# Performance work log

Measured on AMD Instinct MI355X. Metric: run time of the kernel, lower is better.

Reference implementation:

```python
import jax, jax.numpy as jnp
import numpy as np
import math

B, T, D, H = 2, 2048, 1024, 16
DH = D // H

def setup_inputs() -> dict:
    key = jax.random.key(0)
    ks = jax.random.split(key, 7)
    s = 0.02
    return {
        "q": jax.random.normal(ks[0], (B, T, D), jnp.float32),
        "k": jax.random.normal(ks[1], (B, T, D), jnp.float32),
        "v": jax.random.normal(ks[2], (B, T, D), jnp.float32),
        "wq": jax.random.normal(ks[3], (D, D), jnp.float32) * s,
        "wk": jax.random.normal(ks[4], (D, D), jnp.float32) * s,
        "wv": jax.random.normal(ks[5], (D, D), jnp.float32) * s,
        "wo": jax.random.normal(ks[6], (D, D), jnp.float32) * s,
    }

def reference(q, k, v, wq, wk, wv, wo):
    # nn.Linear(bias=False): y = x @ W.T
    qh = (q @ wq.T).reshape(B, T, H, DH).transpose(0, 2, 1, 3)  # [B,H,T,DH]
    kh = (k @ wk.T).reshape(B, T, H, DH).transpose(0, 2, 1, 3)
    vh = (v @ wv.T).reshape(B, T, H, DH).transpose(0, 2, 1, 3)
    scores = jnp.einsum('bhqd,bhkd->bhqk', qh, kh) / math.sqrt(DH)
    # causal mask: disallow j > i
    mask = jnp.triu(jnp.ones((T, T), dtype=bool), k=1)
    scores = jnp.where(mask[None, None], -jnp.inf, scores)
    attn = jax.nn.softmax(scores, axis=-1)  # dropout=0 (eval)
    out = jnp.einsum('bhqk,bhkd->bhqd', attn, vh)
    out = out.transpose(0, 2, 1, 3).reshape(B, T, D)
    return out @ wo.T
```

## Files before the change

kernel.cpp:

```cpp
#include <hip/hip_runtime.h>
#include <cstdint>
#include <cstddef>

#define B_  2
#define T_  2048
#define D_  1024
#define H_  16
#define DH_ 64
#define M_  (B_*T_)

typedef __bf16 bf16x8 __attribute__((ext_vector_type(8)));
typedef float  f32x4  __attribute__((ext_vector_type(4)));
typedef unsigned short us4 __attribute__((ext_vector_type(4)));
typedef unsigned short us8 __attribute__((ext_vector_type(8)));
typedef unsigned short ushort_t;

__device__ __forceinline__ unsigned short f32_to_bf16_rne(float f) {
    unsigned u = __builtin_bit_cast(unsigned, f);
    u += 0x7FFFu + ((u >> 16) & 1u);
    return (unsigned short)(u >> 16);
}

__device__ __forceinline__ void async16(const void* g, void* l) {
    __builtin_amdgcn_global_load_lds(
        (const __attribute__((address_space(1))) unsigned int*)(uintptr_t)g,
        (__attribute__((address_space(3))) unsigned int*)(uintptr_t)l, 16, 0, 0);
}

__global__ __launch_bounds__(256) void cvt_qkv(const float* __restrict__ a, const float* __restrict__ b,
                                               const float* __restrict__ c,
                                               ushort_t* __restrict__ oa, ushort_t* __restrict__ ob,
                                               ushort_t* __restrict__ oc) {
    const float* in = blockIdx.y == 0 ? a : blockIdx.y == 1 ? b : c;
    ushort_t* out   = blockIdx.y == 0 ? oa : blockIdx.y == 1 ? ob : oc;
    int i = (blockIdx.x * 256 + threadIdx.x) * 4;
    float4 f = *reinterpret_cast<const float4*>(in + i);
    us4 o;
    o[0] = f32_to_bf16_rne(f.x); o[1] = f32_to_bf16_rne(f.y);
    o[2] = f32_to_bf16_rne(f.z); o[3] = f32_to_bf16_rne(f.w);
    *reinterpret_cast<us4*>(out + i) = o;
}

__global__ __launch_bounds__(256) void cvt_w(const float* __restrict__ a, const float* __restrict__ b,
                                             const float* __restrict__ c, const float* __restrict__ d,
                                             ushort_t* __restrict__ oa, ushort_t* __restrict__ ob,
                                             ushort_t* __restrict__ oc, ushort_t* __restrict__ od) {
    const float* in = blockIdx.y == 0 ? a : blockIdx.y == 1 ? b : blockIdx.y == 2 ? c : d;
    ushort_t* out   = blockIdx.y == 0 ? oa : blockIdx.y == 1 ? ob : blockIdx.y == 2 ? oc : od;
    int i = (blockIdx.x * 256 + threadIdx.x) * 4;
    float4 f = *reinterpret_cast<const float4*>(in + i);
    us4 o;
    o[0] = f32_to_bf16_rne(f.x); o[1] = f32_to_bf16_rne(f.y);
    o[2] = f32_to_bf16_rne(f.z); o[3] = f32_to_bf16_rne(f.w);
    *reinterpret_cast<us4*>(out + i) = o;
}

__device__ __forceinline__ void gemm_mainloop(const ushort_t* __restrict__ A,
                                              const ushort_t* __restrict__ W,
                                              ushort_t* As, ushort_t* Bs,
                                              int m0, int n0, f32x4 acc[4][4]) {
    const int tid  = threadIdx.x;
    const int lc   = tid & 15;
    const int quad = (tid >> 4) & 3;
    const int wave = tid >> 6;
    const int wm = (wave >> 1) * 64, wn = (wave & 1) * 64;

    const f32x4 fzero = {0.f, 0.f, 0.f, 0.f};
#pragma unroll
    for (int mt = 0; mt < 4; ++mt)
#pragma unroll
        for (int nt = 0; nt < 4; ++nt) acc[mt][nt] = fzero;

    for (int kk = 0; kk < D_; kk += 32) {
        __syncthreads();
#pragma unroll
        for (int i = 0; i < 2; ++i) {
            const int j = i * 256 + tid;
            async16(A + (size_t)(m0 + (j >> 2)) * D_ + kk + (j & 3) * 8, As + j * 8);
            async16(W + (size_t)(n0 + (j >> 2)) * D_ + kk + (j & 3) * 8, Bs + j * 8);
        }
        __syncthreads();
        bf16x8 af[4], bw[4];
#pragma unroll
        for (int mt = 0; mt < 4; ++mt)
            af[mt] = *reinterpret_cast<const bf16x8*>(As + (wm + mt * 16 + lc) * 32 + quad * 8);
#pragma unroll
        for (int nt = 0; nt < 4; ++nt)
            bw[nt] = *reinterpret_cast<const bf16x8*>(Bs + (wn + nt * 16 + lc) * 32 + quad * 8);
#pragma unroll
        for (int mt = 0; mt < 4; ++mt)
#pragma unroll
            for (int nt = 0; nt < 4; ++nt)
                acc[mt][nt] = __builtin_amdgcn_mfma_f32_16x16x32_bf16(af[mt], bw[nt], acc[mt][nt], 0, 0, 0);
    }
}

__global__ __launch_bounds__(256, 2) void gemm_qkv(
    const ushort_t* __restrict__ qb, const ushort_t* __restrict__ kb, const ushort_t* __restrict__ vb,
    const ushort_t* __restrict__ wqb, const ushort_t* __restrict__ wkb, const ushort_t* __restrict__ wvb,
    ushort_t* __restrict__ qhb, ushort_t* __restrict__ khb, ushort_t* __restrict__ vtb) {
    __shared__ __align__(16) ushort_t As[128 * 32];
    __shared__ __align__(16) ushort_t Bs[128 * 32];
    __shared__ __align__(16) ushort_t Ts[4][64 * 16];

    const int z = blockIdx.z;
    const ushort_t* A = z == 0 ? qb : z == 1 ? kb : vb;
    const ushort_t* W = z == 0 ? wqb : z == 1 ? wkb : wvb;
    const int m0 = blockIdx.y * 128, n0 = blockIdx.x * 128;

    f32x4 acc[4][4];
    gemm_mainloop(A, W, As, Bs, m0, n0, acc);

    const int tid = threadIdx.x, lane = tid & 63, lc = tid & 15;
    const int quad = (tid >> 4) & 3, wave = tid >> 6;
    const int wm = (wave >> 1) * 64, wn = (wave & 1) * 64;

    if (z < 2) {
        ushort_t* outp = z == 0 ? qhb : khb;
#pragma unroll
        for (int mt = 0; mt < 4; ++mt)
#pragma unroll
            for (int nt = 0; nt < 4; ++nt)
#pragma unroll
                for (int r = 0; r < 4; ++r) {
                    const int m = m0 + wm + mt * 16 + quad * 4 + r;
                    const int n = n0 + wn + nt * 16 + lc;
                    const int bb = m >> 11, t = m & (T_ - 1);
                    const int hh = n >> 6,  d = n & 63;
                    outp[(((size_t)bb * H_ + hh) * T_ + t) * DH_ + d] = f32_to_bf16_rne(acc[mt][nt][r]);
                }
    } else {
        const int mG = m0 + wm;
        const int bb = mG >> 11, t0 = mG & (T_ - 1);
        const int nG = n0 + wn, hh = nG >> 6;
        ushort_t* base = vtb + ((size_t)bb * H_ + hh) * DH_ * T_;
#pragma unroll
        for (int mt = 0; mt < 4; ++mt) {
#pragma unroll
            for (int nt = 0; nt < 4; ++nt)
#pragma unroll
                for (int r = 0; r < 4; ++r)
                    Ts[wave][(nt * 16 + lc) * 16 + quad * 4 + r] = f32_to_bf16_rne(acc[mt][nt][r]);
#pragma unroll
            for (int it = 0; it < 2; ++it) {
                const int c = it * 64 + lane;
                const int nl = c >> 1, mh = c & 1;
                us8 vv = *reinterpret_cast<const us8*>(Ts[wave] + c * 8);
                *reinterpret_cast<us8*>(base + (size_t)nl * T_ + t0 + mt * 16 + mh * 8) = vv;
            }
        }
    }
}

__global__ __launch_bounds__(256, 2) void gemm_wo(const ushort_t* __restrict__ A,
                                                  const ushort_t* __restrict__ W,
                                                  float* __restrict__ out) {
    __shared__ __align__(16) ushort_t As[128 * 32];
    __shared__ __align__(16) ushort_t Bs[128 * 32];
    const int m0 = blockIdx.y * 128, n0 = blockIdx.x * 128;
    f32x4 acc[4][4];
    gemm_mainloop(A, W, As, Bs, m0, n0, acc);

    const int tid = threadIdx.x, lc = tid & 15;
    const int quad = (tid >> 4) & 3, wave = tid >> 6;
    const int wm = (wave >> 1) * 64, wn = (wave & 1) * 64;
#pragma unroll
    for (int mt = 0; mt < 4; ++mt)
#pragma unroll
        for (int nt = 0; nt < 4; ++nt)
#pragma unroll
            for (int r = 0; r < 4; ++r) {
                const int m = m0 + wm + mt * 16 + quad * 4 + r;
                const int n = n0 + wn + nt * 16 + lc;
                out[(size_t)m * D_ + n] = acc[mt][nt][r];
            }
}

__global__ __launch_bounds__(256, 2) void attn2(const ushort_t* __restrict__ Qh,
                                                const ushort_t* __restrict__ Kh,
                                                const ushort_t* __restrict__ Vt,
                                                ushort_t* __restrict__ Ao) {
    __shared__ __align__(16) ushort_t Ks[2][64 * 64];
    __shared__ __align__(16) ushort_t Vs[2][64 * 64];
    __shared__ __align__(16) ushort_t Ps[4][16 * 72];

    const int tid = threadIdx.x, lane = tid & 63, lc = tid & 15;
    const int quad = (tid >> 4) & 3, wave = tid >> 6;
    const int bh = blockIdx.y, bb = bh >> 4, hh = bh & 15;

    const ushort_t* Qp = Qh + (size_t)bh * T_ * DH_;
    const ushort_t* Kp = Kh + (size_t)bh * T_ * DH_;
    const ushort_t* Vp = Vt + (size_t)bh * DH_ * T_;
    const float SC2 = 0.18033688f;

    auto stage = [&](int buf, int kt) {
        const int k0s = kt * 64;
#pragma unroll
        for (int i = 0; i < 2; ++i) {
            const int j = i * 256 + tid;
            async16(Kp + (size_t)(k0s + (j >> 3)) * DH_ + (j & 7) * 8, Ks[buf] + j * 8);
            async16(Vp + (size_t)(j >> 3) * T_ + k0s + (j & 7) * 8,    Vs[buf] + j * 8);
        }
    };

    const f32x4 fzero = {0.f, 0.f, 0.f, 0.f};

    for (int pass = 0; pass < 2; ++pass) {
        const int qt = pass ? (31 - (int)blockIdx.x) : (int)blockIdx.x;
        const int q0 = qt * 64, nkt = qt + 1;
        const int mbase = q0 + wave * 16;

        const ushort_t* qrow = Qp + (size_t)(mbase + lc) * DH_ + quad * 8;
        bf16x8 aq0 = *reinterpret_cast<const bf16x8*>(qrow);
        bf16x8 aq1 = *reinterpret_cast<const bf16x8*>(qrow + 32);

        f32x4 o[4];
        float lsum[4];
#pragma unroll
        for (int ct = 0; ct < 4; ++ct) o[ct] = fzero;
#pragma unroll
        for (int r = 0; r < 4; ++r) lsum[r] = 0.f;

        __syncthreads();
        stage(0, 0);

        for (int kt = 0; kt < nkt; ++kt) {
            const int cur = kt & 1;
            __syncthreads();
            if (kt + 1 < nkt) stage(cur ^ 1, kt + 1);
            const int k0 = kt * 64;

            f32x4 s[4];
#pragma unroll
            for (int ct = 0; ct < 4; ++ct) {
                const ushort_t* kr = Ks[cur] + (ct * 16 + lc) * 64 + quad * 8;
                bf16x8 bk0 = *reinterpret_cast<const bf16x8*>(kr);
                bf16x8 bk1 = *reinterpret_cast<const bf16x8*>(kr + 32);
                s[ct] = __builtin_amdgcn_mfma_f32_16x16x32_bf16(aq0, bk0, fzero, 0, 0, 0);
                s[ct] = __builtin_amdgcn_mfma_f32_16x16x32_bf16(aq1, bk1, s[ct], 0, 0, 0);
            }

#pragma unroll
            for (int ct = 0; ct < 4; ++ct) {
                const int col = k0 + ct * 16 + lc;
#pragma unroll
                for (int r = 0; r < 4; ++r) {
                    const int row = mbase + quad * 4 + r;
                    const float e = (col <= row) ? __builtin_amdgcn_exp2f(s[ct][r] * SC2) : 0.f;
                    lsum[r] += e;
                    Ps[wave][(quad * 4 + r) * 72 + ct * 16 + lc] = f32_to_bf16_rne(e);
                }
            }
            bf16x8 ap0 = *reinterpret_cast<const bf16x8*>(Ps[wave] + lc * 72 + quad * 8);
            bf16x8 ap1 = *reinterpret_cast<const bf16x8*>(Ps[wave] + lc * 72 + 32 + quad * 8);

#pragma unroll
            for (int ct = 0; ct < 4; ++ct) {
                const ushort_t* vr = Vs[cur] + (ct * 16 + lc) * 64 + quad * 8;
                bf16x8 bv0 = *reinterpret_cast<const bf16x8*>(vr);
                bf16x8 bv1 = *reinterpret_cast<const bf16x8*>(vr + 32);
                o[ct] = __builtin_amdgcn_mfma_f32_16x16x32_bf16(ap0, bv0, o[ct], 0, 0, 0);
                o[ct] = __builtin_amdgcn_mfma_f32_16x16x32_bf16(ap1, bv1, o[ct], 0, 0, 0);
            }
        }

        float inv[4];
#pragma unroll
        for (int r = 0; r < 4; ++r) {
            float l = lsum[r];
#pragma unroll
            for (int d = 1; d < 16; d <<= 1) l += __shfl_xor(l, d);
            inv[r] = 1.0f / l;
        }
#pragma unroll
        for (int ct = 0; ct < 4; ++ct)
#pragma unroll
            for (int r = 0; r < 4; ++r) {
                const int rowq = mbase + quad * 4 + r;
                Ao[((size_t)bb * T_ + rowq) * D_ + hh * DH_ + ct * 16 + lc] =
                    f32_to_bf16_rne(o[ct][r] * inv[r]);
            }
    }
}

extern "C" void kernel_launch(void* const* d_in, const int* in_sizes, int n_in,
                              void* d_out, int out_size, void* d_ws, size_t ws_size,
                              hipStream_t stream) {
    const float* q  = (const float*)d_in[0];
    const float* k  = (const float*)d_in[1];
    const float* v  = (const float*)d_in[2];
    const float* wq = (const float*)d_in[3];
    const float* wk = (const float*)d_in[4];
    const float* wv = (const float*)d_in[5];
    const float* wo = (const float*)d_in[6];

    char* ws = (char*)d_ws;
    size_t off = 0;
    auto alloc = [&](size_t bytes) -> char* {
        char* p = ws + off;
        off += (bytes + 255) & ~(size_t)255;
        return p;
    };
    ushort_t* qb  = (ushort_t*)alloc((size_t)M_ * D_ * 2);
    ushort_t* kb  = (ushort_t*)alloc((size_t)M_ * D_ * 2);
    ushort_t* vb  = (ushort_t*)alloc((size_t)M_ * D_ * 2);
    ushort_t* wqb = (ushort_t*)alloc((size_t)D_ * D_ * 2);
    ushort_t* wkb = (ushort_t*)alloc((size_t)D_ * D_ * 2);
    ushort_t* wvb = (ushort_t*)alloc((size_t)D_ * D_ * 2);
    ushort_t* wob = (ushort_t*)alloc((size_t)D_ * D_ * 2);
    ushort_t* qhb = (ushort_t*)alloc((size_t)M_ * D_ * 2);
    ushort_t* khb = (ushort_t*)alloc((size_t)M_ * D_ * 2);
    ushort_t* vtb = (ushort_t*)alloc((size_t)M_ * D_ * 2);
    ushort_t* aob = (ushort_t*)alloc((size_t)M_ * D_ * 2);

    cvt_qkv<<<dim3(4096, 3), 256, 0, stream>>>(q, k, v, qb, kb, vb);
    cvt_w  <<<dim3(1024, 4), 256, 0, stream>>>(wq, wk, wv, wo, wqb, wkb, wvb, wob);

    gemm_qkv<<<dim3(8, 32, 3), 256, 0, stream>>>(qb, kb, vb, wqb, wkb, wvb, qhb, khb, vtb);

    attn2<<<dim3(16, 32), 256, 0, stream>>>(qhb, khb, vtb, aob);

    gemm_wo<<<dim3(8, 32), 256, 0, stream>>>(aob, wob, (float*)d_out);
}
```

Before: 223.6 us.

## Widen GEMM K-tile with XOR swizzle, split attention KV across wave groups

The two conversion kernels are merged into one launch, with an early exit for the smaller weight tensors. The GEMM main loop stages K=64 per iteration into XOR-swizzled LDS to cut barriers and bank conflicts, and the launch-bound occupancy hint is raised to 3. Attention now uses 512-thread blocks in which two groups of four waves each process alternate KV tiles from a paired double buffer. Their partial outputs and row sums are combined through shared memory at the end, and the P scratch is swizzled too. The cost is more LDS per block, an extra reduction step, and idle work for one group when the tile count is odd.

```diff
diff --git a/kernel.cpp b/kernel.cpp
--- a/kernel.cpp
+++ b/kernel.cpp
@@ -27,27 +27,21 @@
         (__attribute__((address_space(3))) unsigned int*)(uintptr_t)l, 16, 0, 0);
 }
 
-__global__ __launch_bounds__(256) void cvt_qkv(const float* __restrict__ a, const float* __restrict__ b,
-                                               const float* __restrict__ c,
-                                               ushort_t* __restrict__ oa, ushort_t* __restrict__ ob,
-                                               ushort_t* __restrict__ oc) {
-    const float* in = blockIdx.y == 0 ? a : blockIdx.y == 1 ? b : c;
-    ushort_t* out   = blockIdx.y == 0 ? oa : blockIdx.y == 1 ? ob : oc;
+__global__ __launch_bounds__(256) void cvt_all(
+    const float* __restrict__ i0, const float* __restrict__ i1, const float* __restrict__ i2,
+    const float* __restrict__ i3, const float* __restrict__ i4, const float* __restrict__ i5,
+    const float* __restrict__ i6,
+    ushort_t* __restrict__ o0, ushort_t* __restrict__ o1, ushort_t* __restrict__ o2,
+    ushort_t* __restrict__ o3, ushort_t* __restrict__ o4, ushort_t* __restrict__ o5,
+    ushort_t* __restrict__ o6) {
+    const int y = blockIdx.y;
+    const float* in = y == 0 ? i0 : y == 1 ? i1 : y == 2 ? i2 : y == 3 ? i3
+                    : y == 4 ? i4 : y == 5 ? i5 : i6;
+    ushort_t* out  = y == 0 ? o0 : y == 1 ? o1 : y == 2 ? o2 : y == 3 ? o3
+                    : y == 4 ? o4 : y == 5 ? o5 : o6;
+    const int n = (y < 3) ? (M_ * D_) : (D_ * D_);
     int i = (blockIdx.x * 256 + threadIdx.x) * 4;
-    float4 f = *reinterpret_cast<const float4*>(in + i);
-    us4 o;
-    o[0] = f32_to_bf16_rne(f.x); o[1] = f32_to_bf16_rne(f.y);
-    o[2] = f32_to_bf16_rne(f.z); o[3] = f32_to_bf16_rne(f.w);
-    *reinterpret_cast<us4*>(out + i) = o;
-}
-
-__global__ __launch_bounds__(256) void cvt_w(const float* __restrict__ a, const float* __restrict__ b,
-                                             const float* __restrict__ c, const float* __restrict__ d,
-                                             ushort_t* __restrict__ oa, ushort_t* __restrict__ ob,
-                                             ushort_t* __restrict__ oc, ushort_t* __restrict__ od) {
-    const float* in = blockIdx.y == 0 ? a : blockIdx.y == 1 ? b : blockIdx.y == 2 ? c : d;
-    ushort_t* out   = blockIdx.y == 0 ? oa : blockIdx.y == 1 ? ob : blockIdx.y == 2 ? oc : od;
-    int i = (blockIdx.x * 256 + threadIdx.x) * 4;
+    if (i >= n) return;
     float4 f = *reinterpret_cast<const float4*>(in + i);
     us4 o;
     o[0] = f32_to_bf16_rne(f.x); o[1] = f32_to_bf16_rne(f.y);
@@ -64,6 +58,7 @@
     const int quad = (tid >> 4) & 3;
     const int wave = tid >> 6;
     const int wm = (wave >> 1) * 64, wn = (wave & 1) * 64;
+    const int sw = lc & 7;
 
     const f32x4 fzero = {0.f, 0.f, 0.f, 0.f};
 #pragma unroll
@@ -71,36 +66,42 @@
 #pragma unroll
         for (int nt = 0; nt < 4; ++nt) acc[mt][nt] = fzero;
 
-    for (int kk = 0; kk < D_; kk += 32) {
-        __syncthreads();
-#pragma unroll
-        for (int i = 0; i < 2; ++i) {
+    for (int kk = 0; kk < D_; kk += 64) {
+        __syncthreads();
+#pragma unroll
+        for (int i = 0; i < 4; ++i) {
             const int j = i * 256 + tid;
-            async16(A + (size_t)(m0 + (j >> 2)) * D_ + kk + (j & 3) * 8, As + j * 8);
-            async16(W + (size_t)(n0 + (j >> 2)) * D_ + kk + (j & 3) * 8, Bs + j * 8);
-        }
-        __syncthreads();
-        bf16x8 af[4], bw[4];
-#pragma unroll
-        for (int mt = 0; mt < 4; ++mt)
-            af[mt] = *reinterpret_cast<const bf16x8*>(As + (wm + mt * 16 + lc) * 32 + quad * 8);
-#pragma unroll
-        for (int nt = 0; nt < 4; ++nt)
-            bw[nt] = *reinterpret_cast<const bf16x8*>(Bs + (wn + nt * 16 + lc) * 32 + quad * 8);
-#pragma unroll
-        for (int mt = 0; mt < 4; ++mt)
+            const int r = j >> 3, c = (j & 7) ^ (r & 7);
+            async16(A + (size_t)(m0 + r) * D_ + kk + c * 8, As + j * 8);
+            async16(W + (size_t)(n0 + r) * D_ + kk + c * 8, Bs + j * 8);
+        }
+        __syncthreads();
+#pragma unroll
+        for (int ks = 0; ks < 2; ++ks) {
+            bf16x8 af[4], bw[4];
+#pragma unroll
+            for (int mt = 0; mt < 4; ++mt)
+                af[mt] = *reinterpret_cast<const bf16x8*>(
+                    As + (wm + mt * 16 + lc) * 64 + (((ks * 4 + quad) ^ sw) * 8));
 #pragma unroll
             for (int nt = 0; nt < 4; ++nt)
-                acc[mt][nt] = __builtin_amdgcn_mfma_f32_16x16x32_bf16(af[mt], bw[nt], acc[mt][nt], 0, 0, 0);
+                bw[nt] = *reinterpret_cast<const bf16x8*>(
+                    Bs + (wn + nt * 16 + lc) * 64 + (((ks * 4 + quad) ^ sw) * 8));
+#pragma unroll
+            for (int mt = 0; mt < 4; ++mt)
+#pragma unroll
+                for (int nt = 0; nt < 4; ++nt)
+                    acc[mt][nt] = __builtin_amdgcn_mfma_f32_16x16x32_bf16(af[mt], bw[nt], acc[mt][nt], 0, 0, 0);
+        }
     }
 }
 
-__global__ __launch_bounds__(256, 2) void gemm_qkv(
+__global__ __launch_bounds__(256, 3) void gemm_qkv(
     const ushort_t* __restrict__ qb, const ushort_t* __restrict__ kb, const ushort_t* __restrict__ vb,
     const ushort_t* __restrict__ wqb, const ushort_t* __restrict__ wkb, const ushort_t* __restrict__ wvb,
     ushort_t* __restrict__ qhb, ushort_t* __restrict__ khb, ushort_t* __restrict__ vtb) {
-    __shared__ __align__(16) ushort_t As[128 * 32];
-    __shared__ __align__(16) ushort_t Bs[128 * 32];
+    __shared__ __align__(16) ushort_t As[128 * 64];
+    __shared__ __align__(16) ushort_t Bs[128 * 64];
     __shared__ __align__(16) ushort_t Ts[4][64 * 16];
 
     const int z = blockIdx.z;
@@ -152,11 +153,11 @@
     }
 }
 
-__global__ __launch_bounds__(256, 2) void gemm_wo(const ushort_t* __restrict__ A,
+__global__ __launch_bounds__(256, 3) void gemm_wo(const ushort_t* __restrict__ A,
                                                   const ushort_t* __restrict__ W,
                                                   float* __restrict__ out) {
-    __shared__ __align__(16) ushort_t As[128 * 32];
-    __shared__ __align__(16) ushort_t Bs[128 * 32];
+    __shared__ __align__(16) ushort_t As[128 * 64];
+    __shared__ __align__(16) ushort_t Bs[128 * 64];
     const int m0 = blockIdx.y * 128, n0 = blockIdx.x * 128;
     f32x4 acc[4][4];
     gemm_mainloop(A, W, As, Bs, m0, n0, acc);
@@ -176,39 +177,31 @@
             }
 }
 
-__global__ __launch_bounds__(256, 2) void attn2(const ushort_t* __restrict__ Qh,
+__global__ __launch_bounds__(512, 4) void attn3(const ushort_t* __restrict__ Qh,
                                                 const ushort_t* __restrict__ Kh,
                                                 const ushort_t* __restrict__ Vt,
                                                 ushort_t* __restrict__ Ao) {
-    __shared__ __align__(16) ushort_t Ks[2][64 * 64];
-    __shared__ __align__(16) ushort_t Vs[2][64 * 64];
-    __shared__ __align__(16) ushort_t Ps[4][16 * 72];
+    __shared__ __align__(16) ushort_t smem[40960];
 
     const int tid = threadIdx.x, lane = tid & 63, lc = tid & 15;
     const int quad = (tid >> 4) & 3, wave = tid >> 6;
+    const int grp = wave >> 2, sub = wave & 3;
+    const int sw = lc & 7;
     const int bh = blockIdx.y, bb = bh >> 4, hh = bh & 15;
 
     const ushort_t* Qp = Qh + (size_t)bh * T_ * DH_;
     const ushort_t* Kp = Kh + (size_t)bh * T_ * DH_;
     const ushort_t* Vp = Vt + (size_t)bh * DH_ * T_;
     const float SC2 = 0.18033688f;
-
-    auto stage = [&](int buf, int kt) {
-        const int k0s = kt * 64;
-#pragma unroll
-        for (int i = 0; i < 2; ++i) {
-            const int j = i * 256 + tid;
-            async16(Kp + (size_t)(k0s + (j >> 3)) * DH_ + (j & 7) * 8, Ks[buf] + j * 8);
-            async16(Vp + (size_t)(j >> 3) * T_ + k0s + (j & 7) * 8,    Vs[buf] + j * 8);
-        }
-    };
-
     const f32x4 fzero = {0.f, 0.f, 0.f, 0.f};
+
+    ushort_t* Pw = smem + 32768 + wave * 1024;
 
     for (int pass = 0; pass < 2; ++pass) {
         const int qt = pass ? (31 - (int)blockIdx.x) : (int)blockIdx.x;
         const int q0 = qt * 64, nkt = qt + 1;
-        const int mbase = q0 + wave * 16;
+        const int nIt = (nkt + 1) >> 1;
+        const int mbase = q0 + sub * 16;
 
         const ushort_t* qrow = Qp + (size_t)(mbase + lc) * DH_ + quad * 8;
         bf16x8 aq0 = *reinterpret_cast<const bf16x8*>(qrow);
@@ -221,65 +214,100 @@
 #pragma unroll
         for (int r = 0; r < 4; ++r) lsum[r] = 0.f;
 
-        __syncthreads();
-        stage(0, 0);
-
-        for (int kt = 0; kt < nkt; ++kt) {
-            const int cur = kt & 1;
+        auto stagePair = [&](int buf, int kt0) {
+            const int l = tid, r = l >> 3, c = (l & 7) ^ (r & 7);
+            ushort_t* Kd0 = smem + (buf * 2 + 0) * 4096;
+            ushort_t* Kd1 = smem + (buf * 2 + 1) * 4096;
+            ushort_t* Vd0 = smem + 16384 + (buf * 2 + 0) * 4096;
+            ushort_t* Vd1 = smem + 16384 + (buf * 2 + 1) * 4096;
+            if (kt0 < nkt)     async16(Kp + (size_t)(kt0 * 64 + r) * DH_ + c * 8,       Kd0 + l * 8);
+            if (kt0 + 1 < nkt) async16(Kp + (size_t)((kt0 + 1) * 64 + r) * DH_ + c * 8, Kd1 + l * 8);
+            if (kt0 < nkt)     async16(Vp + (size_t)r * T_ + kt0 * 64 + c * 8,          Vd0 + l * 8);
+            if (kt0 + 1 < nkt) async16(Vp + (size_t)r * T_ + (kt0 + 1) * 64 + c * 8,    Vd1 + l * 8);
+        };
+
+        __syncthreads();
+        stagePair(0, 0);
+
+        for (int it = 0; it < nIt; ++it) {
+            const int buf = it & 1;
             __syncthreads();
-            if (kt + 1 < nkt) stage(cur ^ 1, kt + 1);
-            const int k0 = kt * 64;
-
-            f32x4 s[4];
-#pragma unroll
-            for (int ct = 0; ct < 4; ++ct) {
-                const ushort_t* kr = Ks[cur] + (ct * 16 + lc) * 64 + quad * 8;
-                bf16x8 bk0 = *reinterpret_cast<const bf16x8*>(kr);
-                bf16x8 bk1 = *reinterpret_cast<const bf16x8*>(kr + 32);
-                s[ct] = __builtin_amdgcn_mfma_f32_16x16x32_bf16(aq0, bk0, fzero, 0, 0, 0);
-                s[ct] = __builtin_amdgcn_mfma_f32_16x16x32_bf16(aq1, bk1, s[ct], 0, 0, 0);
+            if (it + 1 < nIt) stagePair(buf ^ 1, 2 * (it + 1));
+
+            const int kt = 2 * it + grp;
+            if (kt < nkt) {
+                const int k0 = kt * 64;
+                const ushort_t* Kt = smem + (buf * 2 + grp) * 4096;
+                const ushort_t* Vtile = smem + 16384 + (buf * 2 + grp) * 4096;
+
+                f32x4 s[4];
+#pragma unroll
+                for (int ct = 0; ct < 4; ++ct) {
+                    const ushort_t* kr = Kt + (ct * 16 + lc) * 64;
+                    bf16x8 bk0 = *reinterpret_cast<const bf16x8*>(kr + ((quad ^ sw) * 8));
+                    bf16x8 bk1 = *reinterpret_cast<const bf16x8*>(kr + (((4 + quad) ^ sw) * 8));
+                    s[ct] = __builtin_amdgcn_mfma_f32_16x16x32_bf16(aq0, bk0, fzero, 0, 0, 0);
+                    s[ct] = __builtin_amdgcn_mfma_f32_16x16x32_bf16(aq1, bk1, s[ct], 0, 0, 0);
+                }
+
+#pragma unroll
+                for (int ct = 0; ct < 4; ++ct) {
+                    const int col = k0 + ct * 16 + lc;
+#pragma unroll
+                    for (int r = 0; r < 4; ++r) {
+                        const int row = mbase + quad * 4 + r;
+                        const float e = (col <= row) ? __builtin_amdgcn_exp2f(s[ct][r] * SC2) : 0.f;
+                        lsum[r] += e;
+                        const int prow = quad * 4 + r, pcol = ct * 16 + lc;
+                        Pw[prow * 64 + (((pcol >> 3) ^ (prow & 7)) * 8) + (pcol & 7)] = f32_to_bf16_rne(e);
+                    }
+                }
+                bf16x8 ap0 = *reinterpret_cast<const bf16x8*>(Pw + lc * 64 + ((quad ^ sw) * 8));
+                bf16x8 ap1 = *reinterpret_cast<const bf16x8*>(Pw + lc * 64 + (((4 + quad) ^ sw) * 8));
+
+#pragma unroll
+                for (int ct = 0; ct < 4; ++ct) {
+                    const ushort_t* vr = Vtile + (ct * 16 + lc) * 64;
+                    bf16x8 bv0 = *reinterpret_cast<const bf16x8*>(vr + ((quad ^ sw) * 8));
+                    bf16x8 bv1 = *reinterpret_cast<const bf16x8*>(vr + (((4 + quad) ^ sw) * 8));
+                    o[ct] = __builtin_amdgcn_mfma_f32_16x16x32_bf16(ap0, bv0, o[ct], 0, 0, 0);
+                    o[ct] = __builtin_amdgcn_mfma_f32_16x16x32_bf16(ap1, bv1, o[ct], 0, 0, 0);
+                }
             }
-
-#pragma unroll
-            for (int ct = 0; ct < 4; ++ct) {
-                const int col = k0 + ct * 16 + lc;
+        }
+
+        __syncthreads();
+        float* Osh = (float*)smem;
+        float* Lsh = (float*)(smem + 16384);
+        if (grp == 0) {
+#pragma unroll
+            for (int ct = 0; ct < 4; ++ct)
+#pragma unroll
+                for (int r = 0; r < 4; ++r)
+                    Osh[sub * 1024 + (quad * 4 + r) * 64 + ct * 16 + lc] = o[ct][r];
+#pragma unroll
+            for (int r = 0; r < 4; ++r) Lsh[sub * 256 + lane * 4 + r] = lsum[r];
+        }
+        __syncthreads();
+        if (grp == 1) {
+            float inv[4];
+#pragma unroll
+            for (int r = 0; r < 4; ++r) {
+                float l = lsum[r] + Lsh[sub * 256 + lane * 4 + r];
+#pragma unroll
+                for (int d = 1; d < 16; d <<= 1) l += __shfl_xor(l, d);
+                inv[r] = 1.0f / l;
+            }
+#pragma unroll
+            for (int ct = 0; ct < 4; ++ct)
 #pragma unroll
                 for (int r = 0; r < 4; ++r) {
-                    const int row = mbase + quad * 4 + r;
-                    const float e = (col <= row) ? __builtin_amdgcn_exp2f(s[ct][r] * SC2) : 0.f;
-                    lsum[r] += e;
-                    Ps[wave][(quad * 4 + r) * 72 + ct * 16 + lc] = f32_to_bf16_rne(e);
-                }
-            }
-            bf16x8 ap0 = *reinterpret_cast<const bf16x8*>(Ps[wave] + lc * 72 + quad * 8);
-            bf16x8 ap1 = *reinterpret_cast<const bf16x8*>(Ps[wave] + lc * 72 + 32 + quad * 8);
-
-#pragma unroll
-            for (int ct = 0; ct < 4; ++ct) {
-                const ushort_t* vr = Vs[cur] + (ct * 16 + lc) * 64 + quad * 8;
-                bf16x8 bv0 = *reinterpret_cast<const bf16x8*>(vr);
-                bf16x8 bv1 = *reinterpret_cast<const bf16x8*>(vr + 32);
-                o[ct] = __builtin_amdgcn_mfma_f32_16x16x32_bf16(ap0, bv0, o[ct], 0, 0, 0);
-                o[ct] = __builtin_amdgcn_mfma_f32_16x16x32_bf16(ap1, bv1, o[ct], 0, 0, 0);
-            }
-        }
-
-        float inv[4];
-#pragma unroll
-        for (int r = 0; r < 4; ++r) {
-            float l = lsum[r];
-#pragma unroll
-            for (int d = 1; d < 16; d <<= 1) l += __shfl_xor(l, d);
-            inv[r] = 1.0f / l;
-        }
-#pragma unroll
-        for (int ct = 0; ct < 4; ++ct)
-#pragma unroll
-            for (int r = 0; r < 4; ++r) {
-                const int rowq = mbase + quad * 4 + r;
-                Ao[((size_t)bb * T_ + rowq) * D_ + hh * DH_ + ct * 16 + lc] =
-                    f32_to_bf16_rne(o[ct][r] * inv[r]);
-            }
+                    const float ov = o[ct][r] + Osh[sub * 1024 + (quad * 4 + r) * 64 + ct * 16 + lc];
+                    const int rowq = mbase + quad * 4 + r;
+                    Ao[((size_t)bb * T_ + rowq) * D_ + hh * DH_ + ct * 16 + lc] =
+                        f32_to_bf16_rne(ov * inv[r]);
+                }
+        }
     }
 }
 
@@ -313,12 +341,12 @@
     ushort_t* vtb = (ushort_t*)alloc((size_t)M_ * D_ * 2);
     ushort_t* aob = (ushort_t*)alloc((size_t)M_ * D_ * 2);
 
-    cvt_qkv<<<dim3(4096, 3), 256, 0, stream>>>(q, k, v, qb, kb, vb);
-    cvt_w  <<<dim3(1024, 4), 256, 0, stream>>>(wq, wk, wv, wo, wqb, wkb, wvb, wob);
+    cvt_all<<<dim3(4096, 7), 256, 0, stream>>>(q, k, v, wq, wk, wv, wo,
+                                               qb, kb, vb, wqb, wkb, wvb, wob);
 
     gemm_qkv<<<dim3(8, 32, 3), 256, 0, stream>>>(qb, kb, vb, wqb, wkb, wvb, qhb, khb, vtb);
 
-    attn2<<<dim3(16, 32), 256, 0, stream>>>(qhb, khb, vtb, aob);
+    attn3<<<dim3(16, 32), 512, 0, stream>>>(qhb, khb, vtb, aob);
 
     gemm_wo<<<dim3(8, 32), 256, 0, stream>>>(aob, wob, (float*)d_out);
 }
```

Result: faster. 209.1 us (-6.5%).
